# Kernel tuning notes

Measured on AMD Instinct MI355X. Metric: run time of the kernel, lower is better.

The kernel has to match this reference:

```python
import jax, jax.numpy as jnp
import numpy as np

B, S, DIN, E, M, L = 16, 4096, 64, 512, 128, 4


def _phi(u, R):
    # u: [B,S,E] (already scaled by E**-0.25), R: [E,M]
    logits = u @ R - 0.5 * jnp.sum(u * u, axis=-1, keepdims=True)
    logits = logits - jax.lax.stop_gradient(jnp.max(logits))  # constant shift cancels in num/den ratio
    return jnp.exp(logits) / np.sqrt(M).astype(np.float32)


def setup_inputs() -> dict:
    key = jax.random.key(0)
    ks = jax.random.split(key, 32)
    n = jax.random.normal
    d = {
        'x': n(ks[0], (B, S, DIN), jnp.float32),
        'Wi': n(ks[1], (DIN, E)) / np.sqrt(DIN),
        'bi': jnp.zeros((E,)),
        'pos': n(ks[2], (S, E)) * 0.02,
        'Wq': n(ks[3], (L, E, E)) / np.sqrt(E),
        'bq': jnp.zeros((L, E)),
        'Wk': n(ks[4], (L, E, E)) / np.sqrt(E),
        'bk': jnp.zeros((L, E)),
        'Wv': n(ks[5], (L, E, E)) / np.sqrt(E),
        'bv': jnp.zeros((L, E)),
        'Wo': n(ks[6], (L, E, E)) / np.sqrt(E),
        'bo': jnp.zeros((L, E)),
        'R': n(ks[7], (L, E, M)),
        'ln_g': jnp.ones((L, E)),
        'ln_b': jnp.zeros((L, E)),
        'W1': n(ks[8], (L, E, 4 * E)) / np.sqrt(E),
        'b1': jnp.zeros((L, 4 * E)),
        'W2': n(ks[9], (L, 4 * E, E)) / np.sqrt(4 * E),
        'b2': jnp.zeros((L, E)),
        'Wr1': n(ks[10], (E, E // 2)) / np.sqrt(E),
        'br1': jnp.zeros((E // 2,)),
        'Wr2': n(ks[11], (E // 2, 1)) / np.sqrt(E // 2),
        'br2': jnp.zeros((1,)),
    }
    return d


def reference(x, Wi, bi, pos, Wq, bq, Wk, bk, Wv, bv, Wo, bo, R, ln_g, ln_b, W1, b1, W2, b2, Wr1, br1, Wr2, br2):
    h = x @ Wi + bi + pos[None, :, :]  # [B,S,E]
    scale = E ** -0.25
    for i in range(L):
        residual = h
        # --- Performer linear attention (non-causal FAVOR+) ---
        q = h @ Wq[i] + bq[i]
        k = h @ Wk[i] + bk[i]
        v = h @ Wv[i] + bv[i]
        pq = _phi(q * scale, R[i])  # [B,S,M]
        pk = _phi(k * scale, R[i])  # [B,S,M]
        kv = jnp.einsum('bsm,bse->bme', pk, v)  # [B,M,E]
        z = jnp.sum(pk, axis=1)                  # [B,M]
        num = jnp.einsum('bsm,bme->bse', pq, kv)
        den = jnp.einsum('bsm,bm->bs', pq, z)[..., None]
        a = (num / (den + 1e-6)) @ Wo[i] + bo[i]
        # --- LayerNorm ---
        mu = jnp.mean(a, axis=-1, keepdims=True)
        var = jnp.var(a, axis=-1, keepdims=True)
        y = (a - mu) * jax.lax.rsqrt(var + 1e-5) * ln_g[i] + ln_b[i]
        # --- FFN (dropout is identity in eval) ---
        ff = jax.nn.gelu(y @ W1[i] + b1[i], approximate=False) @ W2[i] + b2[i]
        h = ff + residual
    pooled = h[:, 0, :]  # [B,E]
    return jax.nn.relu(pooled @ Wr1 + br1) @ Wr2 + br2  # [B,1]
```

## Files before the change

kernel.cpp:

```cpp
#include <hip/hip_runtime.h>
#include <math.h>

static constexpr int  cB   = 16;
static constexpr int  cS   = 4096;
static constexpr int  cDIN = 64;
static constexpr int  cE   = 512;
static constexpr int  cM   = 128;
static constexpr int  cL   = 4;
static constexpr int  cFF  = 2048;
static constexpr int  cHE  = 256;
static constexpr long cNBS = (long)cB * cS;
static constexpr int  cNF  = 1792;

typedef __attribute__((ext_vector_type(8))) short  bf16x8;
typedef __attribute__((ext_vector_type(4))) short  bf16x4;
typedef __attribute__((ext_vector_type(4))) float  f32x4;

typedef const __attribute__((address_space(1))) unsigned int g_u32;
typedef __attribute__((address_space(3))) unsigned int l_u32;

__device__ __forceinline__ float b2f(unsigned short u) {
  union { unsigned int i; float f; } x; x.i = ((unsigned int)u) << 16; return x.f;
}
__device__ __forceinline__ unsigned short f2b(float f) {
  union { float f; unsigned int i; } x; x.f = f;
  unsigned int r = x.i + 0x7FFFu + ((x.i >> 16) & 1u);
  return (unsigned short)(r >> 16);
}

#define PSCALE 0.21022410381342863f
#define PNRM   0.022097086912079608f
#define PINV   0.08838834764831845f

#define FLAG_BIAS    2
#define FLAG_GELU    4
#define FLAG_RES     8
#define FLAG_VT      16
#define FLAG_DEN     32
#define FLAG_RNORM   64
#define FLAG_F32OUT  256
#define FLAG_SPLITK8 512
#define FLAG_ATOMIC  1024
#define FLAG_FUSED   2048
#define FLAG_SWZ     4096

#define GMT 128
#define GNT 128
#define GBK 64


__global__ __launch_bounds__(256, 2)
void gemm_kernel(const unsigned short* __restrict__ A,
                 const unsigned short* __restrict__ Bt,
                 const unsigned short* __restrict__ bias,
                 const unsigned short* __restrict__ Res,
                 const float* __restrict__ aux,
                 float* __restrict__ pmax,
                 void* __restrict__ C,
                 int K, int N, int lda, int ldb, float alpha, int flags,
                 long sA, long sB, long sC)
{
  __shared__ __align__(16) unsigned char sraw[32768];
  unsigned short (*As)[64] = (unsigned short (*)[64])sraw;
  unsigned short (*Bs)[64] = (unsigned short (*)[64])(sraw + 16384);
  unsigned short (*stage)[136] = (unsigned short (*)[136])sraw;

  const int tid  = threadIdx.x;
  const int lane = tid & 63;
  const int wid  = tid >> 6;

  int bx = blockIdx.x, by = blockIdx.y;
  if (flags & FLAG_SWZ) {
    const unsigned lid  = blockIdx.x + gridDim.x * blockIdx.y;
    const unsigned xcd  = lid & 7u;
    const unsigned slot = lid >> 3;
    bx = (int)(xcd * (gridDim.y >> 3) + slot / gridDim.x);
    by = (int)(slot % gridDim.x);
  }

  long zb = blockIdx.z;
  const long zc = blockIdx.z;
  int koff = 0;
  if (flags & FLAG_SPLITK8) { koff = (int)(zb & 7) * K; zb >>= 3; }

  const unsigned short* Ab = A + zb * sA + (long)bx * GMT * lda + koff;
  const unsigned short* Bb = Bt + zb * sB + (long)by * GNT * ldb + koff;

  const int srow  = tid >> 3;
  const int scolG = (((tid & 7) ^ (srow & 7)) << 3);
  const unsigned short* gA = Ab + (long)srow * lda + scolG;
  const unsigned short* gB = Bb + (long)srow * ldb + scolG;
  l_u32* lA = (l_u32*)(sraw + tid * 16);
  l_u32* lB = (l_u32*)(sraw + 16384 + tid * 16);

  const f32x4 fzero = {0.f, 0.f, 0.f, 0.f};
  f32x4 acc[4][4];
#pragma unroll
  for (int i = 0; i < 4; ++i)
#pragma unroll
    for (int j = 0; j < 4; ++j) acc[i][j] = fzero;

  const int wm = (wid >> 1) << 6;
  const int wn = (wid & 1) << 6;
  const int fm = lane & 15;
  const int kqh = lane >> 4;

  const long ka32 = (long)32 * lda, kb32 = (long)32 * ldb;
  for (int k0 = 0; k0 < K; k0 += GBK) {
#pragma unroll
    for (int s = 0; s < 4; ++s) {
      __builtin_amdgcn_global_load_lds((g_u32*)(gA + (long)s * ka32 + k0),
                                       (l_u32*)((__attribute__((address_space(3))) char*)lA + s * 4096), 16, 0, 0);
      __builtin_amdgcn_global_load_lds((g_u32*)(gB + (long)s * kb32 + k0),
                                       (l_u32*)((__attribute__((address_space(3))) char*)lB + s * 4096), 16, 0, 0);
    }
    __syncthreads();

#pragma unroll
    for (int kk = 0; kk < 2; ++kk) {
      bf16x8 af[4], bfv[4];
#pragma unroll
      for (int i = 0; i < 4; ++i) {
        const int ca = ((((kk << 2) | kqh) ^ (fm & 7)) << 3);
        af[i]  = *(const bf16x8*)&As[wm + i * 16 + fm][ca];
        bfv[i] = *(const bf16x8*)&Bs[wn + i * 16 + fm][ca];
      }
#pragma unroll
      for (int i = 0; i < 4; ++i)
#pragma unroll
        for (int j = 0; j < 4; ++j)
          acc[i][j] = __builtin_amdgcn_mfma_f32_16x16x32_bf16(af[i], bfv[j], acc[i][j], 0, 0, 0);
    }
    __syncthreads();
  }

  const int rq = (lane >> 4) << 2;
  const long crow0 = (long)bx * GMT + wm;
  const int  ccol0 = by * GNT + wn;

  long rnoff = 0;
  if (flags & FLAG_FUSED) {
    if (by >= 12) {
      float* Lf  = (float*)Res + (long)(by - 12) * (cNBS * (long)cM);
      float* rmx = (float*)aux + ((long)(by - 12) * 2 + (wn >> 6)) * cNBS;
#pragma unroll
      for (int i = 0; i < 4; ++i)
#pragma unroll
        for (int r = 0; r < 4; ++r) {
          const long rr = crow0 + i * 16 + rq + r;
          float mx = -3.0e38f;
#pragma unroll
          for (int j = 0; j < 4; ++j) {
            const int cc = ccol0 + j * 16 + fm;
            float l = acc[i][j][r] * PSCALE + b2f(bias[cc]);
            mx = fmaxf(mx, l);
            Lf[rr * (long)cM + (cc & (cM - 1))] = l;
          }
          mx = fmaxf(mx, __shfl_xor(mx, 1, 64));
          mx = fmaxf(mx, __shfl_xor(mx, 2, 64));
          mx = fmaxf(mx, __shfl_xor(mx, 4, 64));
          mx = fmaxf(mx, __shfl_xor(mx, 8, 64));
          if (fm == 0) rmx[rr] = mx;
        }
      return;
    }
    if (by < 4) flags = FLAG_BIAS | FLAG_VT;
    else { flags = FLAG_BIAS | FLAG_RNORM; if (by >= 8) rnoff = cNBS; }
  }

  if (flags & FLAG_RNORM) {
#pragma unroll
    for (int i = 0; i < 4; ++i)
#pragma unroll
      for (int r = 0; r < 4; ++r) {
        float s = 0.f;
#pragma unroll
        for (int j = 0; j < 4; ++j) {
          float v = acc[i][j][r] * alpha + b2f(bias[ccol0 + j * 16 + fm]);
          s += v * v;
        }
        s += __shfl_xor(s, 1, 64);
        s += __shfl_xor(s, 2, 64);
        s += __shfl_xor(s, 4, 64);
        s += __shfl_xor(s, 8, 64);
        if (fm == 0)
          unsafeAtomicAdd(&pmax[rnoff + crow0 + i * 16 + rq + r], s);
      }
    return;
  }

  if (flags & FLAG_ATOMIC) {
    float* Cf = (float*)C + zb * sC;
#pragma unroll
    for (int j = 0; j < 4; ++j) {
      const int cc = ccol0 + j * 16 + fm;
#pragma unroll
      for (int i = 0; i < 4; ++i)
#pragma unroll
        for (int r = 0; r < 4; ++r) {
          const long rr = crow0 + i * 16 + rq + r;
          unsafeAtomicAdd(&Cf[rr * (long)N + cc], acc[i][j][r] * alpha);
        }
    }
    return;
  }

  if (flags & FLAG_VT) {
    unsigned short* Cb = (unsigned short*)C;
    const int bb = (bx * GMT) >> 12;
    const long sbase = (long)((bx * GMT) & (cS - 1));
#pragma unroll
    for (int rnd = 0; rnd < 2; ++rnd) {
      if ((wn >> 6) == rnd) {
#pragma unroll
        for (int j = 0; j < 4; ++j) {
          const int cc = ccol0 + j * 16 + fm;
          const float bv = (flags & FLAG_BIAS) ? b2f(bias[cc]) : 0.f;
          const int cl = j * 16 + fm;
#pragma unroll
          for (int i = 0; i < 4; ++i)
#pragma unroll
            for (int r = 0; r < 4; ++r)
              stage[cl][wm + i * 16 + rq + r] = f2b(acc[i][j][r] * alpha + bv);
        }
      }
      __syncthreads();
      {
        const int cl = tid >> 2;
        const int sseg = (tid & 3) << 5;
        const int gcol = by * GNT + rnd * 64 + cl;
        unsigned short* dst = Cb + (long)bb * sC + (long)gcol * cS + sbase + sseg;
#pragma unroll
        for (int t = 0; t < 4; ++t)
          *(bf16x8*)(dst + t * 8) = *(const bf16x8*)&stage[cl][sseg + t * 8];
      }
      __syncthreads();
    }
    return;
  }

  const long rowsPerBatch = (long)gridDim.x * GMT;
#pragma unroll
  for (int j = 0; j < 4; ++j) {
    const int cc = ccol0 + j * 16 + fm;
    const float bv = (flags & FLAG_BIAS) ? b2f(bias[cc]) : 0.f;
#pragma unroll
    for (int i = 0; i < 4; ++i) {
      const long rbase = crow0 + i * 16 + rq;
#pragma unroll
      for (int r = 0; r < 4; ++r) {
        const long rr = rbase + r;
        float v = acc[i][j][r] * alpha;
        if (flags & FLAG_DEN)
          v *= 1.f / (fmaxf(aux[zb * rowsPerBatch + rr], 0.f) + 1e-6f);
        v += bv;
        if (flags & FLAG_GELU) v = 0.5f * v * (1.f + erff(v * 0.7071067811865475f));
        const long idx = zc * sC + rr * (long)N + cc;
        if (flags & FLAG_RES) v += b2f(Res[idx]);
        if (flags & FLAG_F32OUT) ((float*)C)[idx] = v;
        else                     ((unsigned short*)C)[idx] = f2b(v);
      }
    }
  }
}

__global__ void detect_kernel(const unsigned short* __restrict__ lng,
                              int* __restrict__ flag) {
  if (threadIdx.x == 0 && blockIdx.x == 0) flag[0] = (lng[0] == 0) ? 1 : 0;
}

__global__ __launch_bounds__(256) void cvt_kernel(const void* __restrict__ in,
                                                  unsigned short* __restrict__ out,
                                                  long n, const int* __restrict__ flag) {
  long i = (long)blockIdx.x * 256 + threadIdx.x;
  if (i >= n) return;
  if (flag[0]) out[i] = f2b(((const float*)in)[i]);
  else         out[i] = ((const unsigned short*)in)[i];
}

__global__ __launch_bounds__(256) void zero4_kernel(float* __restrict__ p) {
  long i = ((long)blockIdx.x * 256 + threadIdx.x) * 4;
  f32x4 z = {0.f, 0.f, 0.f, 0.f};
  *(f32x4*)&p[i] = z;
}

__global__ __launch_bounds__(256) void addpos_kernel(unsigned short* __restrict__ h,
                                                     const unsigned short* __restrict__ pos) {
  long i = ((long)blockIdx.x * 256 + threadIdx.x) * 8;
  long se = i % ((long)cS * cE);
  bf16x8 v = *(bf16x8*)&h[i];
  bf16x8 p = *(const bf16x8*)&pos[se];
#pragma unroll
  for (int r = 0; r < 8; ++r)
    v[r] = (short)f2b(b2f((unsigned short)v[r]) + b2f((unsigned short)p[r]));
  *(bf16x8*)&h[i] = v;
}

__global__ __launch_bounds__(256) void reduceg_kernel(const float* __restrict__ rmax,
                                                      const float* __restrict__ rnorm2,
                                                      float* __restrict__ partials) {
  __shared__ float sm[4];
  const int b = blockIdx.x;
  const int side = b >> 8;
  const long row = ((long)(b & 255)) * 256 + threadIdx.x;
  const float nrm = PNRM * rnorm2[(side == 0 ? cNBS : 0) + row];
  float v = fmaxf(rmax[((long)side * 2 + 0) * cNBS + row],
                  rmax[((long)side * 2 + 1) * cNBS + row]) - nrm;
#pragma unroll
  for (int off = 32; off >= 1; off >>= 1) v = fmaxf(v, __shfl_down(v, off, 64));
  const int w = threadIdx.x >> 6, lane = threadIdx.x & 63;
  if (lane == 0) sm[w] = v;
  __syncthreads();
  if (threadIdx.x == 0)
    partials[b] = fmaxf(fmaxf(sm[0], sm[1]), fmaxf(sm[2], sm[3]));
}

__global__ __launch_bounds__(256) void reducemax2_kernel(const float* __restrict__ partials,
                                                         float* __restrict__ gmax) {
  __shared__ float sm[8];
  const int tid = threadIdx.x;
  for (int half = 0; half < 2; ++half) {
    float mx = partials[half * 256 + tid];
#pragma unroll
    for (int off = 32; off >= 1; off >>= 1) mx = fmaxf(mx, __shfl_down(mx, off, 64));
    if ((tid & 63) == 0) sm[(half << 2) + (tid >> 6)] = mx;
  }
  __syncthreads();
  if (tid == 0) gmax[0] = fmaxf(fmaxf(sm[0], sm[1]), fmaxf(sm[2], sm[3]));
  if (tid == 1) gmax[1] = fmaxf(fmaxf(sm[4], sm[5]), fmaxf(sm[6], sm[7]));
}

__global__ __launch_bounds__(256) void expq_kernel(const float* __restrict__ lf,
                                                   const float* __restrict__ gmx,
                                                   const float* __restrict__ rn,
                                                   unsigned short* __restrict__ P) {
  long i = ((long)blockIdx.x * 256 + threadIdx.x) * 4;
  const float gm = gmx[0];
  const float nrm = PNRM * rn[i >> 7];
  f32x4 v = *(const f32x4*)&lf[i];
  bf16x4 o;
#pragma unroll
  for (int r = 0; r < 4; ++r)
    o[r] = (short)f2b(__expf(fminf(v[r] - nrm - gm, 0.f)) * PINV);
  *(bf16x4*)&P[i] = o;
}

__global__ __launch_bounds__(256) void expT_kernel(const float* __restrict__ lf,
                                                   const float* __restrict__ gmx,
                                                   const float* __restrict__ rn,
                                                   unsigned short* __restrict__ out) {
  __shared__ unsigned short t[32][33];
  const int b = blockIdx.z;
  const float gm = gmx[0];
  const int bx = blockIdx.x << 5, by = blockIdx.y << 5;
  const int tx = threadIdx.x & 31, ty = threadIdx.x >> 5;
  const float* src = lf + (long)b * cS * cM;
  unsigned short* dst = out + (long)b * cM * cS;
#pragma unroll
  for (int i = ty; i < 32; i += 8) {
    const float nrm = PNRM * rn[(long)b * cS + by + i];
    float l = src[(long)(by + i) * cM + bx + tx];
    t[i][tx] = f2b(__expf(fminf(l - nrm - gm, 0.f)) * PINV);
  }
  __syncthreads();
#pragma unroll
  for (int i = ty; i < 32; i += 8)
    dst[(long)(bx + i) * cS + by + tx] = t[tx][i];
}

__global__ __launch_bounds__(256) void kvcvt_kernel(const float* __restrict__ kvacc,
                                                    unsigned short* __restrict__ kvtb) {
  long i = ((long)blockIdx.x * 256 + threadIdx.x) * 4;
  f32x4 v = *(const f32x4*)&kvacc[i];
  bf16x4 o;
#pragma unroll
  for (int r = 0; r < 4; ++r) o[r] = (short)f2b(v[r]);
  *(bf16x4*)&kvtb[i] = o;
}

__global__ __launch_bounds__(128) void phibias_kernel(const unsigned short* __restrict__ bq,
                                                      const unsigned short* __restrict__ R,
                                                      unsigned short* __restrict__ out,
                                                      float scale, int ldo) {
  const int l = blockIdx.x, m = threadIdx.x;
  const unsigned short* b = bq + (long)l * cE;
  const unsigned short* r = R + (long)l * cE * cM;
  float a = 0.f;
  for (int e = 0; e < cE; ++e) a += b2f(b[e]) * b2f(r[(long)e * cM + m]);
  out[(long)l * ldo + m] = f2b(a * scale);
}

__global__ __launch_bounds__(256) void packb_kernel(const unsigned short* __restrict__ bv,
                                                    const unsigned short* __restrict__ bk,
                                                    const unsigned short* __restrict__ bq,
                                                    const unsigned short* __restrict__ sqk,
                                                    unsigned short* __restrict__ out) {
  const int l = blockIdx.x, t = threadIdx.x;
#pragma unroll
  for (int s = 0; s < 512; s += 256) {
    out[l * cNF + s + t]        = bv[l * 512 + s + t];
    out[l * cNF + 512 + s + t]  = bk[l * 512 + s + t];
    out[l * cNF + 1024 + s + t] = bq[l * 512 + s + t];
  }
  out[l * cNF + 1536 + t] = sqk[l * 256 + t];
}

__global__ __launch_bounds__(256) void zsumt_kernel(const unsigned short* __restrict__ qtb,
                                                    float* __restrict__ z) {
  __shared__ float sred[4];
  const int b = blockIdx.x, m = blockIdx.y, tid = threadIdx.x;
  const unsigned short* p = qtb + ((long)b * cM + m) * cS + (long)tid * 16;
  bf16x8 a = *(const bf16x8*)p;
  bf16x8 c = *(const bf16x8*)(p + 8);
  float s = 0.f;
#pragma unroll
  for (int t = 0; t < 8; ++t) s += b2f((unsigned short)a[t]) + b2f((unsigned short)c[t]);
#pragma unroll
  for (int off = 32; off >= 1; off >>= 1) s += __shfl_down(s, off, 64);
  const int w = tid >> 6, lane = tid & 63;
  if (lane == 0) sred[w] = s;
  __syncthreads();
  if (tid == 0) z[b * cM + m] = sred[0] + sred[1] + sred[2] + sred[3];
}

__global__ __launch_bounds__(256) void den_kernel(const unsigned short* __restrict__ P,
                                                  const float* __restrict__ z,
                                                  float* __restrict__ den) {
  const int w = threadIdx.x >> 6, lane = threadIdx.x & 63;
  const long row = (long)blockIdx.x * 4 + w;
  const float* zb = z + (row >> 12) * cM;
  const unsigned short* p = P + row * cM;
  float d = b2f(p[lane]) * zb[lane] + b2f(p[lane + 64]) * zb[lane + 64];
#pragma unroll
  for (int off = 32; off >= 1; off >>= 1) d += __shfl_down(d, off, 64);
  if (lane == 0) den[row] = d;
}

__global__ __launch_bounds__(256) void ln_kernel(unsigned short* __restrict__ a,
                                                 const unsigned short* __restrict__ g,
                                                 const unsigned short* __restrict__ bb) {
  __shared__ float sred[8];
  const long row = blockIdx.x;
  unsigned short* ar = a + row * cE;
  const int tid = threadIdx.x;
  float v0 = b2f(ar[tid]), v1 = b2f(ar[tid + 256]);
  float s = v0 + v1, sq = v0 * v0 + v1 * v1;
#pragma unroll
  for (int off = 32; off >= 1; off >>= 1) {
    s  += __shfl_down(s, off, 64);
    sq += __shfl_down(sq, off, 64);
  }
  const int w = tid >> 6, lane = tid & 63;
  if (lane == 0) { sred[w] = s; sred[4 + w] = sq; }
  __syncthreads();
  const float st  = sred[0] + sred[1] + sred[2] + sred[3];
  const float sqt = sred[4] + sred[5] + sred[6] + sred[7];
  const float mean = st * (1.f / 512.f);
  const float var  = fmaxf(sqt * (1.f / 512.f) - mean * mean, 0.f);
  const float rstd = rsqrtf(var + 1e-5f);
  ar[tid]       = f2b((v0 - mean) * rstd * b2f(g[tid])       + b2f(bb[tid]));
  ar[tid + 256] = f2b((v1 - mean) * rstd * b2f(g[tid + 256]) + b2f(bb[tid + 256]));
}

__global__ __launch_bounds__(256) void transpose_kernel(const unsigned short* __restrict__ in,
                                                        unsigned short* __restrict__ out,
                                                        int R, int C, long sIn, long sOut) {
  __shared__ unsigned short t[32][33];
  in  += (long)blockIdx.z * sIn;
  out += (long)blockIdx.z * sOut;
  const int bx = blockIdx.x << 5, by = blockIdx.y << 5;
  const int tx = threadIdx.x & 31, ty = threadIdx.x >> 5;
#pragma unroll
  for (int i = ty; i < 32; i += 8) t[i][tx] = in[(long)(by + i) * C + bx + tx];
  __syncthreads();
#pragma unroll
  for (int i = ty; i < 32; i += 8) out[(long)(bx + i) * R + by + tx] = t[tx][i];
}

__global__ __launch_bounds__(256) void head_kernel(const unsigned short* __restrict__ h,
                                                   const unsigned short* __restrict__ Wr1,
                                                   const unsigned short* __restrict__ br1,
                                                   const unsigned short* __restrict__ Wr2,
                                                   const unsigned short* __restrict__ br2,
                                                   void* __restrict__ out,
                                                   const int* __restrict__ flag) {
  __shared__ float pooled[cE];
  __shared__ float red[4];
  const int b = blockIdx.x, tid = threadIdx.x;
  pooled[tid]       = b2f(h[(long)b * cS * cE + tid]);
  pooled[tid + 256] = b2f(h[(long)b * cS * cE + tid + 256]);
  __syncthreads();
  float acc = b2f(br1[tid]);
  for (int e = 0; e < cE; ++e) acc += pooled[e] * b2f(Wr1[e * cHE + tid]);
  acc = fmaxf(acc, 0.f) * b2f(Wr2[tid]);
#pragma unroll
  for (int off = 32; off >= 1; off >>= 1) acc += __shfl_down(acc, off, 64);
  const int w = tid >> 6, lane = tid & 63;
  if (lane == 0) red[w] = acc;
  __syncthreads();
  if (tid == 0) {
    float r = red[0] + red[1] + red[2] + red[3] + b2f(br2[0]);
    if (flag[0]) ((float*)out)[b] = r;
    else         ((unsigned short*)out)[b] = f2b(r);
  }
}

extern "C" void kernel_launch(void* const* d_in, const int* in_sizes, int n_in,
                              void* d_out, int out_size, void* d_ws, size_t ws_size,
                              hipStream_t stream) {
  (void)in_sizes; (void)n_in; (void)out_size;

  char* ws = (char*)d_ws;
  size_t off = 0;
  auto alloc = [&](size_t bytes) -> void* {
    void* p = ws + off;
    off += (bytes + 255) & ~(size_t)255;
    return p;
  };
  unsigned short* h   = (unsigned short*)alloc(cNBS * cE * 2);
  unsigned short* X   = (unsigned short*)alloc(cNBS * cE * 2);
  unsigned short* Y   = (unsigned short*)alloc(cNBS * cE * 2);
  unsigned short* Pb  = (unsigned short*)alloc(cNBS * cM * 2);
  unsigned short* kvtb= (unsigned short*)alloc((long)cB * cM * cE * 2);
  unsigned short* kvotb=(unsigned short*)alloc((long)cB * cE * cM * 2);
  float* kvacc        = (float*)alloc((long)cB * cM * cE * 4);
  float* vec64k       = (float*)alloc(cNBS * 4);
  float* rnorm2       = (float*)alloc(2 * cNBS * 4);
  float* rmax         = (float*)alloc(4 * cNBS * 4);
  float* z            = (float*)alloc(cB * cM * 4);
  float* partials     = (float*)alloc(1024 * 4);
  float* gmaxf        = (float*)alloc(256);
  int*   dflag        = (int*)alloc(256);
  unsigned short* WiT = (unsigned short*)alloc((long)cE * cDIN * 2);
  unsigned short* BigB= (unsigned short*)alloc((long)cL * cNF * cE * 2);
  unsigned short* WoT = (unsigned short*)alloc((long)cL * cE * cE * 2);
  unsigned short* RT  = (unsigned short*)alloc((long)cL * cM * cE * 2);
  unsigned short* W1T = (unsigned short*)alloc((long)cL * cFF * cE * 2);
  unsigned short* W2T = (unsigned short*)alloc((long)cL * cE * cFF * 2);
  unsigned short* sb  = (unsigned short*)alloc(170000 * 2);

  unsigned short* WqB = X;
  unsigned short* WkB = WqB + (long)cL * cE * cE;
  unsigned short* WvB = WkB + (long)cL * cE * cE;
  unsigned short* WoB = WvB + (long)cL * cE * cE;
  unsigned short* RmB = WoB + (long)cL * cE * cE;
  unsigned short* W1B = RmB + (long)cL * cE * cM;
  unsigned short* W2B = W1B + (long)cL * cE * cFF;
  unsigned short* WiB = W2B + (long)cL * cE * cFF;
  unsigned short* xb   = Y;
  unsigned short* posb = Y + cNBS * cDIN;
  unsigned short* biC  = sb;
  unsigned short* bqC  = biC  + 512;
  unsigned short* bkC  = bqC  + 2048;
  unsigned short* bvC  = bkC  + 2048;
  unsigned short* boC  = bvC  + 2048;
  unsigned short* b1C  = boC  + 2048;
  unsigned short* b2C  = b1C  + 8192;
  unsigned short* lngC = b2C  + 2048;
  unsigned short* lnbC = lngC + 2048;
  unsigned short* Wr1C = lnbC + 2048;
  unsigned short* br1C = Wr1C + 131072;
  unsigned short* Wr2C = br1C + 256;
  unsigned short* br2C = Wr2C + 256;
  unsigned short* bqkC  = br2C + 16;
  unsigned short* b1792C = bqkC + cL * 256;

  unsigned short* qtb  = X;
  float* logfX         = (float*)X;
  unsigned short* vtb  = Y;
  unsigned short* ab   = Y;
  unsigned short* u1b  = X;

  if (off > ws_size) return;

  detect_kernel<<<1, 64, 0, stream>>>((const unsigned short*)d_in[13], dflag);
  auto cvt = [&](const void* src, unsigned short* dst, long n) {
    cvt_kernel<<<(unsigned)((n + 255) / 256), 256, 0, stream>>>(src, dst, n, dflag);
  };
  cvt(d_in[0],  xb,   cNBS * cDIN);
  cvt(d_in[1],  WiB,  (long)cDIN * cE);
  cvt(d_in[2],  biC,  cE);
  cvt(d_in[3],  posb, (long)cS * cE);
  cvt(d_in[4],  WqB,  (long)cL * cE * cE);
  cvt(d_in[5],  bqC,  (long)cL * cE);
  cvt(d_in[6],  WkB,  (long)cL * cE * cE);
  cvt(d_in[7],  bkC,  (long)cL * cE);
  cvt(d_in[8],  WvB,  (long)cL * cE * cE);
  cvt(d_in[9],  bvC,  (long)cL * cE);
  cvt(d_in[10], WoB,  (long)cL * cE * cE);
  cvt(d_in[11], boC,  (long)cL * cE);
  cvt(d_in[12], RmB,  (long)cL * cE * cM);
  cvt(d_in[13], lngC, (long)cL * cE);
  cvt(d_in[14], lnbC, (long)cL * cE);
  cvt(d_in[15], W1B,  (long)cL * cE * cFF);
  cvt(d_in[16], b1C,  (long)cL * cFF);
  cvt(d_in[17], W2B,  (long)cL * cFF * cE);
  cvt(d_in[18], b2C,  (long)cL * cE);
  cvt(d_in[19], Wr1C, (long)cE * cHE);
  cvt(d_in[20], br1C, cHE);
  cvt(d_in[21], Wr2C, cHE);
  cvt(d_in[22], br2C, 1);

  typedef const unsigned short* cus;
  auto gemm = [&](const void* A, const void* Bt, const void* bias_,
                  const float* aux_, float* pmax_, void* C,
                  long rows, int K, int N, int lda, int ldb, float alpha, int flags,
                  long sA, long sB, long sC, int batches, const void* Res_ = nullptr) {
    dim3 g((unsigned)(rows / 128), (unsigned)(N / 128), (unsigned)batches);
    gemm_kernel<<<g, dim3(256), 0, stream>>>(
        (const unsigned short*)A, (const unsigned short*)Bt,
        (const unsigned short*)bias_, (const unsigned short*)Res_,
        aux_, pmax_, C, K, N, lda, ldb, alpha, flags, sA, sB, sC);
  };

  transpose_kernel<<<dim3(16, 2, 1), 256, 0, stream>>>(WiB, WiT, cDIN, cE, 0, 0);
  transpose_kernel<<<dim3(16, 16, cL), 256, 0, stream>>>(WvB, BigB, cE, cE, (long)cE * cE, (long)cNF * cE);
  transpose_kernel<<<dim3(16, 16, cL), 256, 0, stream>>>(WkB, BigB + (long)512 * cE, cE, cE, (long)cE * cE, (long)cNF * cE);
  transpose_kernel<<<dim3(16, 16, cL), 256, 0, stream>>>(WqB, BigB + (long)1024 * cE, cE, cE, (long)cE * cE, (long)cNF * cE);
  transpose_kernel<<<dim3(16, 16, cL), 256, 0, stream>>>(WoB, WoT, cE, cE, (long)cE * cE, (long)cE * cE);
  transpose_kernel<<<dim3(4, 16, cL), 256, 0, stream>>>(RmB, RT, cE, cM, (long)cE * cM, (long)cE * cM);
  transpose_kernel<<<dim3(64, 16, cL), 256, 0, stream>>>(W1B, W1T, cE, cFF, (long)cE * cFF, (long)cE * cFF);
  transpose_kernel<<<dim3(16, 64, cL), 256, 0, stream>>>(W2B, W2T, cFF, cE, (long)cFF * cE, (long)cFF * cE);

  gemm(RT, WqB, nullptr, nullptr, nullptr, BigB + (long)1536 * cE, cM, cE, cE, cE, cE, 1.f, 0,
       (long)cM * cE, (long)cE * cE, (long)cNF * cE, cL);
  gemm(RT, WkB, nullptr, nullptr, nullptr, BigB + (long)1664 * cE, cM, cE, cE, cE, cE, 1.f, 0,
       (long)cM * cE, (long)cE * cE, (long)cNF * cE, cL);
  phibias_kernel<<<cL, 128, 0, stream>>>(bqC, RmB, bqkC, PSCALE, 256);
  phibias_kernel<<<cL, 128, 0, stream>>>(bkC, RmB, bqkC + 128, PSCALE, 256);
  packb_kernel<<<cL, 256, 0, stream>>>(bvC, bkC, bqC, bqkC, b1792C);

  gemm(xb, WiT, biC, nullptr, nullptr, h, cNBS, cDIN, cE, cDIN, cDIN, 1.f,
       FLAG_BIAS, 0, 0, 0, 1);
  addpos_kernel<<<16384, 256, 0, stream>>>(h, posb);

  for (int i = 0; i < cL; ++i) {
    cus WoT_i = WoT + (long)i * cE * cE;  cus bo_i = boC + (long)i * cE;
    cus BigB_i = BigB + (long)i * cNF * cE;
    cus b1792_i = b1792C + (long)i * cNF;
    cus g_i   = lngC + (long)i * cE;      cus b_i  = lnbC + (long)i * cE;
    cus W1T_i = W1T + (long)i * cFF * cE; cus b1_i = b1C + (long)i * cFF;
    cus W2T_i = W2T + (long)i * cE * cFF; cus b2_i = b2C + (long)i * cE;

    zero4_kernel<<<128, 256, 0, stream>>>(rnorm2);
    gemm_kernel<<<dim3(14, 512, 1), dim3(256), 0, stream>>>(
        h, BigB_i, b1792_i, (const unsigned short*)logfX, (const float*)rmax,
        rnorm2, vtb, cE, cNF, cE, cE, 1.f, FLAG_FUSED | FLAG_SWZ,
        0, 0, (long)cE * cS);

    reduceg_kernel<<<512, 256, 0, stream>>>(rmax, rnorm2, partials);
    reducemax2_kernel<<<1, 256, 0, stream>>>(partials, gmaxf);
    expq_kernel<<<8192, 256, 0, stream>>>(logfX, gmaxf, rnorm2 + cNBS, Pb);
    expT_kernel<<<dim3(4, 128, cB), 256, 0, stream>>>(logfX + cNBS * cM, gmaxf + 1, rnorm2, qtb);

    zsumt_kernel<<<dim3(cB, cM), 256, 0, stream>>>(qtb, z);
    den_kernel<<<16384, 256, 0, stream>>>(Pb, z, vec64k);

    zero4_kernel<<<1024, 256, 0, stream>>>(kvacc);
    gemm(qtb, vtb, nullptr, nullptr, nullptr, kvacc, cM, cS / 8, cE, cS, cS, 1.f,
         FLAG_SPLITK8 | FLAG_ATOMIC, (long)cM * cS, (long)cE * cS, (long)cM * cE, cB * 8);
    kvcvt_kernel<<<1024, 256, 0, stream>>>(kvacc, kvtb);

    gemm(WoT_i, kvtb, nullptr, nullptr, nullptr, kvotb, cE, cE, cM, cE, cE, 1.f,
         0, 0, (long)cM * cE, (long)cE * cM, cB);

    gemm(Pb, kvotb, bo_i, vec64k, nullptr, ab, cS, cM, cE, cM, cM, 1.f,
         FLAG_DEN | FLAG_BIAS, (long)cS * cM, (long)cE * cM, (long)cS * cE, cB);
    ln_kernel<<<cNBS, 256, 0, stream>>>(ab, g_i, b_i);

    for (int c = 0; c < 4; ++c) {
      const unsigned short* yc = ab + (long)c * 16384 * cE;
      unsigned short* hc = h + (long)c * 16384 * cE;
      gemm_kernel<<<dim3(16, 128, 1), dim3(256), 0, stream>>>(
          yc, W1T_i, b1_i, nullptr, nullptr, nullptr, u1b,
          cE, cFF, cE, cE, 1.f, FLAG_BIAS | FLAG_GELU | FLAG_SWZ, 0, 0, 0);
      gemm_kernel<<<dim3(4, 128, 1), dim3(256), 0, stream>>>(
          u1b, W2T_i, b2_i, hc, nullptr, nullptr, hc,
          cFF, cE, cFF, cFF, 1.f, FLAG_BIAS | FLAG_RES | FLAG_SWZ, 0, 0, 0);
    }
  }

  head_kernel<<<cB, 256, 0, stream>>>(h, Wr1C, br1C, Wr2C, br2C, d_out, dflag);
}
```

Baseline: 3.624 ms.

## Store bf16 exp-normalized features in fused GEMM epilogue and batch input conversions

The fused QKV GEMM epilogue now computes exp(logit - local half-row max) and writes bf16 instead of fp32 logits. The later expq/expT kernels become scale kernels that multiply by a per-row factor built from the row max, norm and global max. This halves intermediate feature traffic and drops one buffer pass. It also merges the 23 separate input conversion launches into one grid-stride kernel, and relies on the exp rescaling staying numerically equivalent in bf16.

```diff
diff --git a/kernel.cpp b/kernel.cpp
--- a/kernel.cpp
+++ b/kernel.cpp
@@ -141,26 +141,31 @@
   long rnoff = 0;
   if (flags & FLAG_FUSED) {
     if (by >= 12) {
-      float* Lf  = (float*)Res + (long)(by - 12) * (cNBS * (long)cM);
+      unsigned short* P = (unsigned short*)Res + (long)(by - 12) * (cNBS * (long)cM);
       float* rmx = (float*)aux + ((long)(by - 12) * 2 + (wn >> 6)) * cNBS;
 #pragma unroll
       for (int i = 0; i < 4; ++i)
 #pragma unroll
         for (int r = 0; r < 4; ++r) {
           const long rr = crow0 + i * 16 + rq + r;
+          float lv[4];
           float mx = -3.0e38f;
 #pragma unroll
           for (int j = 0; j < 4; ++j) {
             const int cc = ccol0 + j * 16 + fm;
-            float l = acc[i][j][r] * PSCALE + b2f(bias[cc]);
-            mx = fmaxf(mx, l);
-            Lf[rr * (long)cM + (cc & (cM - 1))] = l;
+            lv[j] = acc[i][j][r] * PSCALE + b2f(bias[cc]);
+            mx = fmaxf(mx, lv[j]);
           }
           mx = fmaxf(mx, __shfl_xor(mx, 1, 64));
           mx = fmaxf(mx, __shfl_xor(mx, 2, 64));
           mx = fmaxf(mx, __shfl_xor(mx, 4, 64));
           mx = fmaxf(mx, __shfl_xor(mx, 8, 64));
           if (fm == 0) rmx[rr] = mx;
+#pragma unroll
+          for (int j = 0; j < 4; ++j) {
+            const int cc = ccol0 + j * 16 + fm;
+            P[rr * (long)cM + (cc & (cM - 1))] = f2b(__expf(lv[j] - mx));
+          }
         }
       return;
     }
@@ -269,13 +274,20 @@
   if (threadIdx.x == 0 && blockIdx.x == 0) flag[0] = (lng[0] == 0) ? 1 : 0;
 }
 
-__global__ __launch_bounds__(256) void cvt_kernel(const void* __restrict__ in,
-                                                  unsigned short* __restrict__ out,
-                                                  long n, const int* __restrict__ flag) {
-  long i = (long)blockIdx.x * 256 + threadIdx.x;
-  if (i >= n) return;
-  if (flag[0]) out[i] = f2b(((const float*)in)[i]);
-  else         out[i] = ((const unsigned short*)in)[i];
+struct CvtB { const void* s[23]; unsigned short* d[23]; long cum[24]; };
+
+__global__ __launch_bounds__(256) void cvtall_kernel(CvtB b, const int* __restrict__ flag) {
+  const long T = b.cum[23];
+  const int f = flag[0];
+  for (long i = (long)blockIdx.x * 256 + threadIdx.x; i < T;
+       i += (long)gridDim.x * 256) {
+    int t = 0;
+#pragma unroll
+    for (int k = 1; k < 23; ++k) t += (i >= b.cum[k]) ? 1 : 0;
+    const long e = i - b.cum[t];
+    b.d[t][e] = f ? f2b(((const float*)b.s[t])[e])
+                  : ((const unsigned short*)b.s[t])[e];
+  }
 }
 
 __global__ __launch_bounds__(256) void zero4_kernel(float* __restrict__ p) {
@@ -330,42 +342,45 @@
   if (tid == 1) gmax[1] = fmaxf(fmaxf(sm[4], sm[5]), fmaxf(sm[6], sm[7]));
 }
 
-__global__ __launch_bounds__(256) void expq_kernel(const float* __restrict__ lf,
-                                                   const float* __restrict__ gmx,
-                                                   const float* __restrict__ rn,
-                                                   unsigned short* __restrict__ P) {
-  long i = ((long)blockIdx.x * 256 + threadIdx.x) * 4;
+__global__ __launch_bounds__(256) void scaleq_kernel(unsigned short* __restrict__ P,
+                                                     const float* __restrict__ gmx,
+                                                     const float* __restrict__ rmax,
+                                                     const float* __restrict__ rn) {
+  long i = ((long)blockIdx.x * 256 + threadIdx.x) * 8;
   const float gm = gmx[0];
-  const float nrm = PNRM * rn[i >> 7];
-  f32x4 v = *(const f32x4*)&lf[i];
-  bf16x4 o;
-#pragma unroll
-  for (int r = 0; r < 4; ++r)
-    o[r] = (short)f2b(__expf(fminf(v[r] - nrm - gm, 0.f)) * PINV);
-  *(bf16x4*)&P[i] = o;
-}
-
-__global__ __launch_bounds__(256) void expT_kernel(const float* __restrict__ lf,
-                                                   const float* __restrict__ gmx,
-                                                   const float* __restrict__ rn,
-                                                   unsigned short* __restrict__ out) {
+  const long row = i >> 7;
+  const int half = (int)((i >> 6) & 1);
+  const float f = __expf(rmax[(long)half * cNBS + row] - PNRM * rn[row] - gm) * PINV;
+  bf16x8 v = *(bf16x8*)&P[i];
+#pragma unroll
+  for (int r = 0; r < 8; ++r)
+    v[r] = (short)f2b(b2f((unsigned short)v[r]) * f);
+  *(bf16x8*)&P[i] = v;
+}
+
+__global__ __launch_bounds__(256) void scaleT_kernel(const unsigned short* __restrict__ phik,
+                                                     const float* __restrict__ gmx,
+                                                     const float* __restrict__ rmax,
+                                                     const float* __restrict__ rn,
+                                                     unsigned short* __restrict__ out) {
   __shared__ unsigned short t[32][33];
   const int b = blockIdx.z;
   const float gm = gmx[0];
-  const int bx = blockIdx.x << 5, by = blockIdx.y << 5;
+  const int bx = blockIdx.x << 5, byy = blockIdx.y << 5;
   const int tx = threadIdx.x & 31, ty = threadIdx.x >> 5;
-  const float* src = lf + (long)b * cS * cM;
+  const int half = bx >> 6;
+  const unsigned short* src = phik + (long)b * cS * cM;
   unsigned short* dst = out + (long)b * cM * cS;
 #pragma unroll
   for (int i = ty; i < 32; i += 8) {
-    const float nrm = PNRM * rn[(long)b * cS + by + i];
-    float l = src[(long)(by + i) * cM + bx + tx];
-    t[i][tx] = f2b(__expf(fminf(l - nrm - gm, 0.f)) * PINV);
+    const long row = (long)b * cS + byy + i;
+    const float f = __expf(rmax[(long)half * cNBS + row] - PNRM * rn[row] - gm) * PINV;
+    t[i][tx] = f2b(b2f(src[(long)(byy + i) * cM + bx + tx]) * f);
   }
   __syncthreads();
 #pragma unroll
   for (int i = ty; i < 32; i += 8)
-    dst[(long)(bx + i) * cS + by + tx] = t[tx][i];
+    dst[(long)(bx + i) * cS + byy + tx] = t[tx][i];
 }
 
 __global__ __launch_bounds__(256) void kvcvt_kernel(const float* __restrict__ kvacc,
@@ -565,8 +580,9 @@
   unsigned short* bqkC  = br2C + 16;
   unsigned short* b1792C = bqkC + cL * 256;
 
-  unsigned short* qtb  = X;
-  float* logfX         = (float*)X;
+  unsigned short* pq   = X;
+  unsigned short* phik = X + (long)cNBS * cM;
+  unsigned short* qtb  = Pb;
   unsigned short* vtb  = Y;
   unsigned short* ab   = Y;
   unsigned short* u1b  = X;
@@ -574,32 +590,40 @@
   if (off > ws_size) return;
 
   detect_kernel<<<1, 64, 0, stream>>>((const unsigned short*)d_in[13], dflag);
-  auto cvt = [&](const void* src, unsigned short* dst, long n) {
-    cvt_kernel<<<(unsigned)((n + 255) / 256), 256, 0, stream>>>(src, dst, n, dflag);
-  };
-  cvt(d_in[0],  xb,   cNBS * cDIN);
-  cvt(d_in[1],  WiB,  (long)cDIN * cE);
-  cvt(d_in[2],  biC,  cE);
-  cvt(d_in[3],  posb, (long)cS * cE);
-  cvt(d_in[4],  WqB,  (long)cL * cE * cE);
-  cvt(d_in[5],  bqC,  (long)cL * cE);
-  cvt(d_in[6],  WkB,  (long)cL * cE * cE);
-  cvt(d_in[7],  bkC,  (long)cL * cE);
-  cvt(d_in[8],  WvB,  (long)cL * cE * cE);
-  cvt(d_in[9],  bvC,  (long)cL * cE);
-  cvt(d_in[10], WoB,  (long)cL * cE * cE);
-  cvt(d_in[11], boC,  (long)cL * cE);
-  cvt(d_in[12], RmB,  (long)cL * cE * cM);
-  cvt(d_in[13], lngC, (long)cL * cE);
-  cvt(d_in[14], lnbC, (long)cL * cE);
-  cvt(d_in[15], W1B,  (long)cL * cE * cFF);
-  cvt(d_in[16], b1C,  (long)cL * cFF);
-  cvt(d_in[17], W2B,  (long)cL * cFF * cE);
-  cvt(d_in[18], b2C,  (long)cL * cE);
-  cvt(d_in[19], Wr1C, (long)cE * cHE);
-  cvt(d_in[20], br1C, cHE);
-  cvt(d_in[21], Wr2C, cHE);
-  cvt(d_in[22], br2C, 1);
+  {
+    CvtB cb;
+    long len[23];
+    int ix = 0;
+    auto addcv = [&](const void* s_, unsigned short* d_, long n_) {
+      cb.s[ix] = s_; cb.d[ix] = d_; len[ix] = n_; ++ix;
+    };
+    addcv(d_in[0],  xb,   cNBS * cDIN);
+    addcv(d_in[1],  WiB,  (long)cDIN * cE);
+    addcv(d_in[2],  biC,  cE);
+    addcv(d_in[3],  posb, (long)cS * cE);
+    addcv(d_in[4],  WqB,  (long)cL * cE * cE);
+    addcv(d_in[5],  bqC,  (long)cL * cE);
+    addcv(d_in[6],  WkB,  (long)cL * cE * cE);
+    addcv(d_in[7],  bkC,  (long)cL * cE);
+    addcv(d_in[8],  WvB,  (long)cL * cE * cE);
+    addcv(d_in[9],  bvC,  (long)cL * cE);
+    addcv(d_in[10], WoB,  (long)cL * cE * cE);
+    addcv(d_in[11], boC,  (long)cL * cE);
+    addcv(d_in[12], RmB,  (long)cL * cE * cM);
+    addcv(d_in[13], lngC, (long)cL * cE);
+    addcv(d_in[14], lnbC, (long)cL * cE);
+    addcv(d_in[15], W1B,  (long)cL * cE * cFF);
+    addcv(d_in[16], b1C,  (long)cL * cFF);
+    addcv(d_in[17], W2B,  (long)cL * cFF * cE);
+    addcv(d_in[18], b2C,  (long)cL * cE);
+    addcv(d_in[19], Wr1C, (long)cE * cHE);
+    addcv(d_in[20], br1C, cHE);
+    addcv(d_in[21], Wr2C, cHE);
+    addcv(d_in[22], br2C, 1);
+    cb.cum[0] = 0;
+    for (int k = 0; k < 23; ++k) cb.cum[k + 1] = cb.cum[k] + len[k];
+    cvtall_kernel<<<2048, 256, 0, stream>>>(cb, dflag);
+  }
 
   typedef const unsigned short* cus;
   auto gemm = [&](const void* A, const void* Bt, const void* bias_,
@@ -644,17 +668,17 @@
 
     zero4_kernel<<<128, 256, 0, stream>>>(rnorm2);
     gemm_kernel<<<dim3(14, 512, 1), dim3(256), 0, stream>>>(
-        h, BigB_i, b1792_i, (const unsigned short*)logfX, (const float*)rmax,
+        h, BigB_i, b1792_i, (const unsigned short*)pq, (const float*)rmax,
         rnorm2, vtb, cE, cNF, cE, cE, 1.f, FLAG_FUSED | FLAG_SWZ,
         0, 0, (long)cE * cS);
 
     reduceg_kernel<<<512, 256, 0, stream>>>(rmax, rnorm2, partials);
     reducemax2_kernel<<<1, 256, 0, stream>>>(partials, gmaxf);
-    expq_kernel<<<8192, 256, 0, stream>>>(logfX, gmaxf, rnorm2 + cNBS, Pb);
-    expT_kernel<<<dim3(4, 128, cB), 256, 0, stream>>>(logfX + cNBS * cM, gmaxf + 1, rnorm2, qtb);
+    scaleq_kernel<<<4096, 256, 0, stream>>>(pq, gmaxf, rmax, rnorm2 + cNBS);
+    scaleT_kernel<<<dim3(4, 128, cB), 256, 0, stream>>>(phik, gmaxf + 1, rmax + 2 * cNBS, rnorm2, qtb);
 
     zsumt_kernel<<<dim3(cB, cM), 256, 0, stream>>>(qtb, z);
-    den_kernel<<<16384, 256, 0, stream>>>(Pb, z, vec64k);
+    den_kernel<<<16384, 256, 0, stream>>>(pq, z, vec64k);
 
     zero4_kernel<<<1024, 256, 0, stream>>>(kvacc);
     gemm(qtb, vtb, nullptr, nullptr, nullptr, kvacc, cM, cS / 8, cE, cS, cS, 1.f,
@@ -664,7 +688,7 @@
     gemm(WoT_i, kvtb, nullptr, nullptr, nullptr, kvotb, cE, cE, cM, cE, cE, 1.f,
          0, 0, (long)cM * cE, (long)cE * cM, cB);
 
-    gemm(Pb, kvotb, bo_i, vec64k, nullptr, ab, cS, cM, cE, cM, cM, 1.f,
+    gemm(pq, kvotb, bo_i, vec64k, nullptr, ab, cS, cM, cE, cM, cM, 1.f,
          FLAG_DEN | FLAG_BIAS, (long)cS * cM, (long)cE * cM, (long)cS * cE, cB);
     ln_kernel<<<cNBS, 256, 0, stream>>>(ab, g_i, b_i);
 
```

Result: faster. 3.483 ms (-3.9%).
